# Kernel tuning notes

Hardware: AMD Instinct MI355X
Metric: run time of the kernel (lower is better)

## Reference

```python
import jax, jax.numpy as jnp
import numpy as np

B, S, V, H = 32, 512, 32, 128
EPS = 1e-5

def _ln(h, w, b):
    m = jnp.mean(h, axis=-1, keepdims=True)
    var = jnp.mean((h - m) ** 2, axis=-1, keepdims=True)
    return (h - m) * jax.lax.rsqrt(var + EPS) * w + b

def setup_inputs() -> dict:
    key = jax.random.key(0)
    ks = jax.random.split(key, 24)
    n = lambda k, shp: jax.random.normal(k, shp, dtype=jnp.float32) * 0.05
    return {
        "x": jax.random.normal(ks[0], (B, S, V), dtype=jnp.float32),
        # flattened GRN (input_dim=V -> H)
        "fw1": n(ks[1], (H, V)), "fb1": jnp.zeros((H,), jnp.float32),
        "fw2": n(ks[2], (H, H)), "fb2": jnp.zeros((H,), jnp.float32),
        "fgw": n(ks[3], (H, H)), "fgb": jnp.zeros((H,), jnp.float32),
        "fsw": n(ks[4], (H, V)), "fsb": jnp.zeros((H,), jnp.float32),
        "flnw": jnp.ones((H,), jnp.float32), "flnb": jnp.zeros((H,), jnp.float32),
        # V per-variable GRNs (input_dim=1 -> H), stacked on leading V axis
        "vw1": n(ks[5], (V, H)), "vb1": jnp.zeros((V, H), jnp.float32),
        "vw2": n(ks[6], (V, H, H)), "vb2": jnp.zeros((V, H), jnp.float32),
        "vgw": n(ks[7], (V, H, H)), "vgb": jnp.zeros((V, H), jnp.float32),
        "vsw": n(ks[8], (V, H)), "vsb": jnp.zeros((V, H), jnp.float32),
        "vlnw": jnp.ones((V, H), jnp.float32), "vlnb": jnp.zeros((V, H), jnp.float32),
    }

def reference(x, fw1, fb1, fw2, fb2, fgw, fgb, fsw, fsb, flnw, flnb,
              vw1, vb1, vw2, vb2, vgw, vgb, vsw, vsb, vlnw, vlnb):
    # ---- flattened GRN -> variable weights ----
    h = jax.nn.elu(jnp.einsum('bsv,hv->bsh', x, fw1) + fb1)
    h = jnp.einsum('bsh,kh->bsk', h, fw2) + fb2
    g = jax.nn.sigmoid(jnp.einsum('bsh,kh->bsk', h, fgw) + fgb)
    skip = jnp.einsum('bsv,hv->bsh', x, fsw) + fsb
    w_out = _ln(g * h + (1.0 - g) * skip, flnw, flnb)        # [B,S,H]
    weights = jax.nn.softmax(w_out[..., :V], axis=-1)        # [B,S,V]
    # ---- per-variable GRNs, batched over V ----
    xe = x[..., None]                                         # [B,S,V,1]
    hv = jax.nn.elu(xe * vw1 + vb1)                           # [B,S,V,H]
    hv = jnp.einsum('bsvh,vkh->bsvk', hv, vw2) + vb2
    gv = jax.nn.sigmoid(jnp.einsum('bsvh,vkh->bsvk', hv, vgw) + vgb)
    skipv = xe * vsw + vsb                                    # [B,S,V,H]
    vout = _ln(gv * hv + (1.0 - gv) * skipv, vlnw, vlnb)      # [B,S,V,H]
    # ---- softmax-weighted combination ----
    selected = jnp.einsum('bsvh,bsv->bsh', vout, weights)     # [B,S,H]
    return selected, weights
```

## Files before the change

### kernel.cpp

```cpp
#include <hip/hip_runtime.h>
#include <hip/hip_bf16.h>

typedef __bf16 bf16_t;
typedef __bf16 bf16x8 __attribute__((ext_vector_type(8)));
typedef float  f32x4  __attribute__((ext_vector_type(4)));

#define DEVFN static __device__ __forceinline__

constexpr int TOK   = 32 * 512;
constexpr int W_OFF = TOK * 128;

constexpr size_t WS_A_VW2 = 0;
constexpr size_t WS_A_WG2 = (size_t)1 << 20;
constexpr size_t WS_BG2   = (size_t)2 << 20;
constexpr size_t WS_A_FW2 = ((size_t)2 << 20) + (64u  << 10);
constexpr size_t WS_A_WG1 = ((size_t)2 << 20) + (128u << 10);
constexpr size_t WS_BG1   = ((size_t)2 << 20) + (192u << 10);
constexpr size_t WS_A_FW1 = ((size_t)2 << 20) + (224u << 10);
constexpr size_t WS_A_FSW = ((size_t)2 << 20) + (256u << 10);
constexpr size_t WS_PART  = (size_t)3 << 20;
constexpr size_t PART_SZ  = (size_t)TOK * 128 * 4;

DEVFN float eluf(float z)  { return z > 0.0f ? z : (__expf(z) - 1.0f); }
DEVFN float sigmf(float z) { return __builtin_amdgcn_rcpf(1.0f + __expf(-z)); }
DEVFN unsigned short f2bfu(float f){ bf16_t h = (bf16_t)f; return __builtin_bit_cast(unsigned short, h); }

DEVFN uint4 pack8(f32x4 a, f32x4 b){
  uint4 r;
  r.x = (unsigned)f2bfu(a[0]) | ((unsigned)f2bfu(a[1]) << 16);
  r.y = (unsigned)f2bfu(a[2]) | ((unsigned)f2bfu(a[3]) << 16);
  r.z = (unsigned)f2bfu(b[0]) | ((unsigned)f2bfu(b[1]) << 16);
  r.w = (unsigned)f2bfu(b[2]) | ((unsigned)f2bfu(b[3]) << 16);
  return r;
}
DEVFN f32x4 mfma16(bf16x8 a, bf16x8 b, f32x4 c){
  return __builtin_amdgcn_mfma_f32_16x16x32_bf16(a, b, c, 0, 0, 0);
}
DEVFN bf16x8 asbf(uint4 u){ return __builtin_bit_cast(bf16x8, u); }

__global__ void k0_prep(const float* __restrict__ fw1, const float* __restrict__ fw2,
                        const float* __restrict__ fgw, const float* __restrict__ fgb,
                        const float* __restrict__ fb2, const float* __restrict__ fsw,
                        const float* __restrict__ vw2, const float* __restrict__ vgw,
                        const float* __restrict__ vgb, const float* __restrict__ vb2,
                        unsigned char* __restrict__ ws)
{
  const int b = blockIdx.x, tid = threadIdx.x;
  if (b < 256){
    const int v  = b >> 3;
    const int k2 = (b & 7) * 16 + (tid >> 4);
    const int h0 = (tid & 15) * 8;
    const float* gw = vgw + ((size_t)v * 128 + k2) * 128;
    const float* w2 = vw2 + (size_t)v * 128 * 128;
    f32x4 a0 = {0,0,0,0}, a1 = {0,0,0,0};
    for (int k = 0; k < 128; ++k){
      float a = gw[k];
      f32x4 u = *(const f32x4*)(w2 + k*128 + h0);
      f32x4 w = *(const f32x4*)(w2 + k*128 + h0 + 4);
      #pragma unroll
      for (int e = 0; e < 4; ++e){ a0[e] = fmaf(a, u[e], a0[e]); a1[e] = fmaf(a, w[e], a1[e]); }
    }
    unsigned blk = (unsigned)(h0 >> 3) ^ (unsigned)(k2 & 7);
    *(uint4*)(ws + WS_A_WG2 + (size_t)v*32768 + (size_t)k2*256 + blk*16) = pack8(a0, a1);
    if ((b & 7) == 0 && tid < 128){
      const float* gr = vgw + ((size_t)v*128 + tid) * 128;
      const float* vb = vb2 + v*128;
      float s = vgb[v*128 + tid];
      for (int k = 0; k < 128; ++k) s = fmaf(gr[k], vb[k], s);
      ((float*)(ws + WS_BG2))[v*128 + tid] = s;
    }
  } else if (b < 288){
    const int v = b - 256;
    const int k = tid >> 1, hh = (tid & 1) * 64;
    const float* src = vw2 + ((size_t)v*128 + k) * 128;
    #pragma unroll
    for (int i = 0; i < 8; ++i){
      int h0 = hh + i*8;
      f32x4 a = *(const f32x4*)(src + h0);
      f32x4 c = *(const f32x4*)(src + h0 + 4);
      unsigned blk = (unsigned)(h0 >> 3) ^ (unsigned)(k & 7);
      *(uint4*)(ws + WS_A_VW2 + (size_t)v*32768 + (size_t)k*256 + blk*16) = pack8(a, c);
    }
  } else if (b < 296){
    const int k2 = (b - 288) * 16 + (tid >> 4);
    const int h0 = (tid & 15) * 8;
    const float* gw = fgw + (size_t)k2 * 128;
    f32x4 a0 = {0,0,0,0}, a1 = {0,0,0,0};
    for (int k = 0; k < 128; ++k){
      float a = gw[k];
      f32x4 u = *(const f32x4*)(fw2 + k*128 + h0);
      f32x4 w = *(const f32x4*)(fw2 + k*128 + h0 + 4);
      #pragma unroll
      for (int e = 0; e < 4; ++e){ a0[e] = fmaf(a, u[e], a0[e]); a1[e] = fmaf(a, w[e], a1[e]); }
    }
    unsigned blk = (unsigned)(h0 >> 3) ^ (unsigned)(k2 & 7);
    *(uint4*)(ws + WS_A_WG1 + (size_t)k2*256 + blk*16) = pack8(a0, a1);
    if (b == 288 && tid < 128){
      const float* gr = fgw + (size_t)tid * 128;
      float s = fgb[tid];
      for (int k = 0; k < 128; ++k) s = fmaf(gr[k], fb2[k], s);
      ((float*)(ws + WS_BG1))[tid] = s;
    }
  } else if (b == 296){
    const int k = tid >> 1, hh = (tid & 1) * 64;
    const float* src = fw2 + (size_t)k * 128;
    #pragma unroll
    for (int i = 0; i < 8; ++i){
      int h0 = hh + i*8;
      f32x4 a = *(const f32x4*)(src + h0);
      f32x4 c = *(const f32x4*)(src + h0 + 4);
      unsigned blk = (unsigned)(h0 >> 3) ^ (unsigned)(k & 7);
      *(uint4*)(ws + WS_A_FW2 + (size_t)k*256 + blk*16) = pack8(a, c);
    }
  } else if (b == 297){
    const int k = tid >> 1, v0 = (tid & 1) * 16;
    #pragma unroll
    for (int i = 0; i < 2; ++i){
      f32x4 a  = *(const f32x4*)(fw1 + k*32 + v0 + i*8);
      f32x4 c  = *(const f32x4*)(fw1 + k*32 + v0 + i*8 + 4);
      *(uint4*)(ws + WS_A_FW1 + (size_t)k*64 + (size_t)v0*2 + i*16) = pack8(a, c);
      f32x4 a2 = *(const f32x4*)(fsw + k*32 + v0 + i*8);
      f32x4 c2 = *(const f32x4*)(fsw + k*32 + v0 + i*8 + 4);
      *(uint4*)(ws + WS_A_FSW + (size_t)k*64 + (size_t)v0*2 + i*16) = pack8(a2, c2);
    }
  }
}

__global__ __launch_bounds__(256) void k1_flat(
  const float* __restrict__ x,   const float* __restrict__ fb1,
  const float* __restrict__ fb2, const float* __restrict__ fsb,
  const float* __restrict__ flnw,const float* __restrict__ flnb,
  const unsigned char* __restrict__ ws, float* __restrict__ out)
{
  __shared__ __align__(16) unsigned char ldsW[65536];
  __shared__ __align__(16) unsigned char ldsH[4][4096];
  const int tid = threadIdx.x;
  const int wid = tid >> 6, lane = tid & 63;
  const int tl = lane & 15, q = lane >> 4;
  const int t0 = blockIdx.x * 64;
  const int tw = t0 + wid * 16 + tl;

  {
    const uint4* s1 = (const uint4*)(ws + WS_A_FW2);
    const uint4* s2 = (const uint4*)(ws + WS_A_WG1);
    uint4* d1 = (uint4*)ldsW;
    uint4* d2 = (uint4*)(ldsW + 32768);
    #pragma unroll
    for (int i = 0; i < 8; ++i){ d1[tid + i*256] = s1[tid + i*256]; d2[tid + i*256] = s2[tid + i*256]; }
  }
  bf16x8 xf;
  {
    f32x4 a = *(const f32x4*)(x + (size_t)tw*32 + q*8);
    f32x4 c = *(const f32x4*)(x + (size_t)tw*32 + q*8 + 4);
    #pragma unroll
    for (int e = 0; e < 4; ++e){ xf[e] = (bf16_t)a[e]; xf[e+4] = (bf16_t)c[e]; }
  }
  __syncthreads();

  const unsigned swzt = (unsigned)(tl & 7) << 4;
  #pragma unroll
  for (int mt = 0; mt < 8; ++mt){
    const int row = mt*16 + tl;
    uint4 araw = *(const uint4*)(ws + WS_A_FW1 + (size_t)row*64 + q*16);
    f32x4 acc = *(const f32x4*)(fb1 + mt*16 + q*4);
    acc = mfma16(asbf(araw), xf, acc);
    ushort4 hb;
    hb.x = f2bfu(eluf(acc[0])); hb.y = f2bfu(eluf(acc[1]));
    hb.z = f2bfu(eluf(acc[2])); hb.w = f2bfu(eluf(acc[3]));
    *(ushort4*)(ldsH[wid] + (unsigned)tl*256 + (((unsigned)(mt*32 + q*8)) ^ swzt)) = hb;
  }
  bf16x8 h1f[4];
  #pragma unroll
  for (int kb = 0; kb < 4; ++kb)
    h1f[kb] = asbf(*(const uint4*)(ldsH[wid] + (unsigned)tl*256 + (((unsigned)(kb*64 + q*16)) ^ swzt)));

  f32x4 wo[8];
  const float* bg1p = (const float*)(ws + WS_BG1);
  #pragma unroll
  for (int mt = 0; mt < 8; ++mt){
    const int row = mt*16 + tl;
    const uint4* aw = (const uint4*)(ldsW + (size_t)row*256);
    const uint4* ag = (const uint4*)(ldsW + 32768 + (size_t)row*256);
    const unsigned rsw = (unsigned)(row & 7);
    f32x4 h2 = *(const f32x4*)(fb2 + mt*16 + q*4);
    f32x4 gp = *(const f32x4*)(bg1p + mt*16 + q*4);
    #pragma unroll
    for (int kb = 0; kb < 4; ++kb){
      unsigned blk = (unsigned)(kb*4 + q) ^ rsw;
      h2 = mfma16(asbf(aw[blk]), h1f[kb], h2);
      gp = mfma16(asbf(ag[blk]), h1f[kb], gp);
    }
    uint4 asr = *(const uint4*)(ws + WS_A_FSW + (size_t)row*64 + q*16);
    f32x4 sk = *(const f32x4*)(fsb + mt*16 + q*4);
    sk = mfma16(asbf(asr), xf, sk);
    #pragma unroll
    for (int r = 0; r < 4; ++r){
      float g = sigmf(gp[r]);
      wo[mt][r] = sk[r] + g * (h2[r] - sk[r]);
    }
  }
  float sm = 0.f, sq = 0.f;
  #pragma unroll
  for (int mt = 0; mt < 8; ++mt)
  #pragma unroll
  for (int r = 0; r < 4; ++r){ float p = wo[mt][r]; sm += p; sq = fmaf(p, p, sq); }
  sm += __shfl_xor(sm, 16); sm += __shfl_xor(sm, 32);
  sq += __shfl_xor(sq, 16); sq += __shfl_xor(sq, 32);
  const float mean = sm * (1.f/128.f);
  const float var  = sq * (1.f/128.f) - mean*mean;
  const float rs   = __builtin_amdgcn_rsqf(var + 1e-5f);
  float wv[8];
  #pragma unroll
  for (int mt = 0; mt < 2; ++mt){
    f32x4 lw = *(const f32x4*)(flnw + mt*16 + q*4);
    f32x4 lb = *(const f32x4*)(flnb + mt*16 + q*4);
    #pragma unroll
    for (int r = 0; r < 4; ++r) wv[mt*4+r] = (wo[mt][r] - mean) * rs * lw[r] + lb[r];
  }
  float mx = wv[0];
  #pragma unroll
  for (int j = 1; j < 8; ++j) mx = fmaxf(mx, wv[j]);
  mx = fmaxf(mx, __shfl_xor(mx, 16)); mx = fmaxf(mx, __shfl_xor(mx, 32));
  float se = 0.f;
  #pragma unroll
  for (int j = 0; j < 8; ++j){ wv[j] = __expf(wv[j] - mx); se += wv[j]; }
  se += __shfl_xor(se, 16); se += __shfl_xor(se, 32);
  const float inv = __builtin_amdgcn_rcpf(se);
  #pragma unroll
  for (int mt = 0; mt < 2; ++mt)
  #pragma unroll
  for (int r = 0; r < 4; ++r)
    out[(size_t)W_OFF + (size_t)tw*32 + mt*16 + q*4 + r] = wv[mt*4+r] * inv;
}

__global__ __launch_bounds__(512, 2) void k2_main(
  const float* __restrict__ x,   const float* __restrict__ vw1,
  const float* __restrict__ vb1, const float* __restrict__ vb2,
  const float* __restrict__ vsw, const float* __restrict__ vsb,
  const float* __restrict__ vlnw,const float* __restrict__ vlnb,
  const unsigned char* __restrict__ ws, float* __restrict__ out,
  float* __restrict__ part, int nvg)
{
  __shared__ __align__(16) uint4 slab[4096];
  const int tid = threadIdx.x;
  const int wid = tid >> 6, lane = tid & 63;
  const int tl = lane & 15, q = lane >> 4;
  const int bid = blockIdx.x;
  const int c   = bid & 127;
  const int g   = bid >> 7;
  const int VPG = 32 / nvg;
  const int vbase = g * VPG;
  const int t0 = ((c & 7) * 16 + (c >> 3)) * 128;
  const int ta = t0 + wid * 16 + tl;
  const float* bg2p = (const float*)(ws + WS_BG2);
  float* __restrict__ dst = (g == nvg - 1) ? out : (part + (size_t)g * TOK * 128);

  {
    const uint4* sa = (const uint4*)(ws + WS_A_VW2 + (size_t)vbase*32768);
    const uint4* sg = (const uint4*)(ws + WS_A_WG2 + (size_t)vbase*32768);
    #pragma unroll
    for (int i = 0; i < 4; ++i) slab[tid + i*512] = sa[tid + i*512];
    #pragma unroll
    for (int i = 0; i < 4; ++i) slab[2048 + tid + i*512] = sg[tid + i*512];
  }
  __syncthreads();

  f32x4 sel[8];
  #pragma unroll
  for (int mt = 0; mt < 8; ++mt) sel[mt] = (f32x4){0.f,0.f,0.f,0.f};

  for (int vi = 0; vi < VPG; ++vi){
    const int v = vbase + vi;
    const float xv0 = x[(size_t)ta*32 + v];
    const float wt0 = out[(size_t)W_OFF + (size_t)ta*32 + v];

    bf16x8 bf0[4];
    #pragma unroll
    for (int kb = 0; kb < 4; ++kb){
      const float* wp = vw1 + v*128 + kb*32 + q*8;
      const float* bp = vb1 + v*128 + kb*32 + q*8;
      f32x4 w0v = *(const f32x4*)wp, w1v = *(const f32x4*)(wp + 4);
      f32x4 b0v = *(const f32x4*)bp, b1v = *(const f32x4*)(bp + 4);
      bf16x8 f0;
      #pragma unroll
      for (int e = 0; e < 4; ++e){
        f0[e]   = (bf16_t)eluf(fmaf(xv0, w0v[e], b0v[e]));
        f0[e+4] = (bf16_t)eluf(fmaf(xv0, w1v[e], b1v[e]));
      }
      bf0[kb] = f0;
    }

    f32x4 pre[8];
    #pragma unroll
    for (int mt = 0; mt < 8; ++mt){
      const int row = mt*16 + tl;
      const uint4* arow = slab + row*16;
      const uint4* grow = slab + 2048 + row*16;
      const unsigned rsw = (unsigned)(row & 7);
      f32x4 h0 = *(const f32x4*)(vb2 + v*128 + mt*16 + q*4);
      f32x4 g0 = *(const f32x4*)(bg2p + v*128 + mt*16 + q*4);
      #pragma unroll
      for (int kb = 0; kb < 4; ++kb){
        const unsigned blk = (unsigned)(kb*4 + q) ^ rsw;
        h0 = mfma16(asbf(arow[blk]), bf0[kb], h0);
        g0 = mfma16(asbf(grow[blk]), bf0[kb], g0);
      }
      f32x4 sw_ = *(const f32x4*)(vsw + v*128 + mt*16 + q*4);
      f32x4 sb_ = *(const f32x4*)(vsb + v*128 + mt*16 + q*4);
      #pragma unroll
      for (int r = 0; r < 4; ++r){
        float sk0 = fmaf(xv0, sw_[r], sb_[r]);
        pre[mt][r] = sk0 + sigmf(g0[r]) * (h0[r] - sk0);
      }
    }

    {
      float sm = 0.f, sq = 0.f;
      #pragma unroll
      for (int mt = 0; mt < 8; ++mt)
      #pragma unroll
      for (int r = 0; r < 4; ++r){ float p = pre[mt][r]; sm += p; sq = fmaf(p, p, sq); }
      sm += __shfl_xor(sm, 16); sm += __shfl_xor(sm, 32);
      sq += __shfl_xor(sq, 16); sq += __shfl_xor(sq, 32);
      const float mean = sm * (1.f/128.f);
      const float var  = sq * (1.f/128.f) - mean*mean;
      const float rsq  = __builtin_amdgcn_rsqf(var + 1e-5f);
      const float c1   = wt0 * rsq;
      #pragma unroll
      for (int mt = 0; mt < 8; ++mt){
        f32x4 lw = *(const f32x4*)(vlnw + v*128 + mt*16 + q*4);
        f32x4 lb = *(const f32x4*)(vlnb + v*128 + mt*16 + q*4);
        #pragma unroll
        for (int r = 0; r < 4; ++r)
          sel[mt][r] = fmaf((pre[mt][r] - mean) * lw[r], c1,
                            fmaf(wt0, lb[r], sel[mt][r]));
      }
    }

    __syncthreads();
    if (vi + 1 < VPG){
      const uint4* sa = (const uint4*)(ws + WS_A_VW2 + (size_t)(v+1)*32768);
      const uint4* sg = (const uint4*)(ws + WS_A_WG2 + (size_t)(v+1)*32768);
      #pragma unroll
      for (int i = 0; i < 4; ++i) slab[tid + i*512] = sa[tid + i*512];
      #pragma unroll
      for (int i = 0; i < 4; ++i) slab[2048 + tid + i*512] = sg[tid + i*512];
      __syncthreads();
    }
  }

  #pragma unroll
  for (int mt = 0; mt < 8; ++mt)
    *(f32x4*)(dst + (size_t)ta*128 + mt*16 + q*4) = sel[mt];
}

__global__ __launch_bounds__(256) void k3_reduce(float* __restrict__ out,
                                                 const float* __restrict__ part,
                                                 int nparts)
{
  const size_t idx = (size_t)blockIdx.x * 256 + threadIdx.x;
  f32x4 s = ((const f32x4*)out)[idx];
  for (int g = 0; g < nparts; ++g){
    f32x4 p = ((const f32x4*)part)[(size_t)g * TOK * 32 + idx];
    #pragma unroll
    for (int r = 0; r < 4; ++r) s[r] += p[r];
  }
  ((f32x4*)out)[idx] = s;
}

extern "C" void kernel_launch(void* const* d_in, const int* in_sizes, int n_in,
                              void* d_out, int out_size, void* d_ws, size_t ws_size,
                              hipStream_t stream)
{
  (void)in_sizes; (void)n_in; (void)out_size;
  const float* x    = (const float*)d_in[0];
  const float* fw1  = (const float*)d_in[1];
  const float* fb1  = (const float*)d_in[2];
  const float* fw2  = (const float*)d_in[3];
  const float* fb2  = (const float*)d_in[4];
  const float* fgw  = (const float*)d_in[5];
  const float* fgb  = (const float*)d_in[6];
  const float* fsw  = (const float*)d_in[7];
  const float* fsb  = (const float*)d_in[8];
  const float* flnw = (const float*)d_in[9];
  const float* flnb = (const float*)d_in[10];
  const float* vw1  = (const float*)d_in[11];
  const float* vb1  = (const float*)d_in[12];
  const float* vw2  = (const float*)d_in[13];
  const float* vb2  = (const float*)d_in[14];
  const float* vgw  = (const float*)d_in[15];
  const float* vgb  = (const float*)d_in[16];
  const float* vsw  = (const float*)d_in[17];
  const float* vsb  = (const float*)d_in[18];
  const float* vlnw = (const float*)d_in[19];
  const float* vlnb = (const float*)d_in[20];
  float* out = (float*)d_out;
  unsigned char* ws = (unsigned char*)d_ws;
  float* part = (float*)(ws + WS_PART);

  k0_prep<<<298, 256, 0, stream>>>(fw1, fw2, fgw, fgb, fb2, fsw, vw2, vgw, vgb, vb2, ws);
  k1_flat<<<256, 256, 0, stream>>>(x, fb1, fb2, fsb, flnw, flnb, ws, out);

  if (ws_size >= WS_PART + 3 * PART_SZ){
    k2_main<<<512, 512, 0, stream>>>(x, vw1, vb1, vb2, vsw, vsb, vlnw, vlnb,
                                     ws, out, part, 4);
    k3_reduce<<<2048, 256, 0, stream>>>(out, part, 3);
  } else if (ws_size >= WS_PART + PART_SZ){
    k2_main<<<256, 512, 0, stream>>>(x, vw1, vb1, vb2, vsw, vsb, vlnw, vlnb,
                                     ws, out, part, 2);
    k3_reduce<<<2048, 256, 0, stream>>>(out, part, 1);
  } else {
    k2_main<<<128, 512, 0, stream>>>(x, vw1, vb1, vb2, vsw, vsb, vlnw, vlnb,
                                     ws, out, part, 1);
  }
}
```

Before: 141.3 us.

## Double-buffer weight slabs via async global-to-LDS loads, process two token tiles per wave

```diff
diff --git a/kernel.cpp b/kernel.cpp
--- a/kernel.cpp
+++ b/kernel.cpp
@@ -233,7 +233,7 @@
     out[(size_t)W_OFF + (size_t)tw*32 + mt*16 + q*4 + r] = wv[mt*4+r] * inv;
 }
 
-__global__ __launch_bounds__(512, 2) void k2_main(
+__global__ __launch_bounds__(512, 1) void k2_main(
   const float* __restrict__ x,   const float* __restrict__ vw1,
   const float* __restrict__ vb1, const float* __restrict__ vb2,
   const float* __restrict__ vsw, const float* __restrict__ vsb,
@@ -241,117 +241,138 @@
   const unsigned char* __restrict__ ws, float* __restrict__ out,
   float* __restrict__ part, int nvg)
 {
-  __shared__ __align__(16) uint4 slab[4096];
+  __shared__ __align__(16) uint4 slab[8192];
   const int tid = threadIdx.x;
   const int wid = tid >> 6, lane = tid & 63;
   const int tl = lane & 15, q = lane >> 4;
   const int bid = blockIdx.x;
-  const int c   = bid & 127;
-  const int g   = bid >> 7;
+  const int c   = bid & 63;
+  const int g   = bid >> 6;
   const int VPG = 32 / nvg;
   const int vbase = g * VPG;
-  const int t0 = ((c & 7) * 16 + (c >> 3)) * 128;
-  const int ta = t0 + wid * 16 + tl;
+  const int t0 = ((c & 7) * 8 + (c >> 3)) * 256;
+  const int ta = t0 + wid * 32 + tl, tb = ta + 16;
   const float* bg2p = (const float*)(ws + WS_BG2);
   float* __restrict__ dst = (g == nvg - 1) ? out : (part + (size_t)g * TOK * 128);
 
-  {
-    const uint4* sa = (const uint4*)(ws + WS_A_VW2 + (size_t)vbase*32768);
-    const uint4* sg = (const uint4*)(ws + WS_A_WG2 + (size_t)vbase*32768);
-    #pragma unroll
-    for (int i = 0; i < 4; ++i) slab[tid + i*512] = sa[tid + i*512];
-    #pragma unroll
-    for (int i = 0; i < 4; ++i) slab[2048 + tid + i*512] = sg[tid + i*512];
-  }
+  auto stage = [&](int buf, int v){
+    const uint4* sa = (const uint4*)(ws + WS_A_VW2 + (size_t)v*32768) + tid;
+    const uint4* sg = (const uint4*)(ws + WS_A_WG2 + (size_t)v*32768) + tid;
+    uint4* da = slab + buf*4096 + tid;
+    uint4* dg = slab + buf*4096 + 2048 + tid;
+    #pragma unroll
+    for (int i = 0; i < 4; ++i)
+      __builtin_amdgcn_global_load_lds(
+        (const __attribute__((address_space(1))) void*)(sa + i*512),
+        (__attribute__((address_space(3))) void*)(da + i*512), 16, 0, 0);
+    #pragma unroll
+    for (int i = 0; i < 4; ++i)
+      __builtin_amdgcn_global_load_lds(
+        (const __attribute__((address_space(1))) void*)(sg + i*512),
+        (__attribute__((address_space(3))) void*)(dg + i*512), 16, 0, 0);
+  };
+
+  stage(0, vbase);
   __syncthreads();
 
-  f32x4 sel[8];
-  #pragma unroll
-  for (int mt = 0; mt < 8; ++mt) sel[mt] = (f32x4){0.f,0.f,0.f,0.f};
-
+  f32x4 sel[2][8];
+  #pragma unroll
+  for (int mt = 0; mt < 8; ++mt){ sel[0][mt] = (f32x4){0,0,0,0}; sel[1][mt] = (f32x4){0,0,0,0}; }
+
+  int cur = 0;
   for (int vi = 0; vi < VPG; ++vi){
     const int v = vbase + vi;
+    if (vi + 1 < VPG) stage(cur ^ 1, v + 1);
+
     const float xv0 = x[(size_t)ta*32 + v];
+    const float xv1 = x[(size_t)tb*32 + v];
     const float wt0 = out[(size_t)W_OFF + (size_t)ta*32 + v];
-
-    bf16x8 bf0[4];
+    const float wt1 = out[(size_t)W_OFF + (size_t)tb*32 + v];
+
+    bf16x8 bf0[4], bf1[4];
     #pragma unroll
     for (int kb = 0; kb < 4; ++kb){
       const float* wp = vw1 + v*128 + kb*32 + q*8;
       const float* bp = vb1 + v*128 + kb*32 + q*8;
       f32x4 w0v = *(const f32x4*)wp, w1v = *(const f32x4*)(wp + 4);
       f32x4 b0v = *(const f32x4*)bp, b1v = *(const f32x4*)(bp + 4);
-      bf16x8 f0;
+      bf16x8 f0, f1;
       #pragma unroll
       for (int e = 0; e < 4; ++e){
         f0[e]   = (bf16_t)eluf(fmaf(xv0, w0v[e], b0v[e]));
         f0[e+4] = (bf16_t)eluf(fmaf(xv0, w1v[e], b1v[e]));
+        f1[e]   = (bf16_t)eluf(fmaf(xv1, w0v[e], b0v[e]));
+        f1[e+4] = (bf16_t)eluf(fmaf(xv1, w1v[e], b1v[e]));
       }
-      bf0[kb] = f0;
-    }
-
-    f32x4 pre[8];
+      bf0[kb] = f0; bf1[kb] = f1;
+    }
+
+    const uint4* sl = slab + cur*4096;
+    f32x4 pre[8][2];
     #pragma unroll
     for (int mt = 0; mt < 8; ++mt){
       const int row = mt*16 + tl;
-      const uint4* arow = slab + row*16;
-      const uint4* grow = slab + 2048 + row*16;
+      const uint4* arow = sl + row*16;
+      const uint4* grow = sl + 2048 + row*16;
       const unsigned rsw = (unsigned)(row & 7);
-      f32x4 h0 = *(const f32x4*)(vb2 + v*128 + mt*16 + q*4);
-      f32x4 g0 = *(const f32x4*)(bg2p + v*128 + mt*16 + q*4);
+      f32x4 bini = *(const f32x4*)(vb2 + v*128 + mt*16 + q*4);
+      f32x4 gini = *(const f32x4*)(bg2p + v*128 + mt*16 + q*4);
+      f32x4 h0 = bini, h1 = bini, g0 = gini, g1 = gini;
       #pragma unroll
       for (int kb = 0; kb < 4; ++kb){
         const unsigned blk = (unsigned)(kb*4 + q) ^ rsw;
-        h0 = mfma16(asbf(arow[blk]), bf0[kb], h0);
-        g0 = mfma16(asbf(grow[blk]), bf0[kb], g0);
+        bf16x8 a = asbf(arow[blk]);
+        bf16x8 gg = asbf(grow[blk]);
+        h0 = mfma16(a, bf0[kb], h0);
+        h1 = mfma16(a, bf1[kb], h1);
+        g0 = mfma16(gg, bf0[kb], g0);
+        g1 = mfma16(gg, bf1[kb], g1);
       }
       f32x4 sw_ = *(const f32x4*)(vsw + v*128 + mt*16 + q*4);
       f32x4 sb_ = *(const f32x4*)(vsb + v*128 + mt*16 + q*4);
       #pragma unroll
       for (int r = 0; r < 4; ++r){
         float sk0 = fmaf(xv0, sw_[r], sb_[r]);
-        pre[mt][r] = sk0 + sigmf(g0[r]) * (h0[r] - sk0);
+        float sk1 = fmaf(xv1, sw_[r], sb_[r]);
+        pre[mt][0][r] = sk0 + sigmf(g0[r]) * (h0[r] - sk0);
+        pre[mt][1][r] = sk1 + sigmf(g1[r]) * (h1[r] - sk1);
       }
     }
 
-    {
+    #pragma unroll
+    for (int nt = 0; nt < 2; ++nt){
+      const float wt = nt ? wt1 : wt0;
       float sm = 0.f, sq = 0.f;
       #pragma unroll
       for (int mt = 0; mt < 8; ++mt)
       #pragma unroll
-      for (int r = 0; r < 4; ++r){ float p = pre[mt][r]; sm += p; sq = fmaf(p, p, sq); }
+      for (int r = 0; r < 4; ++r){ float p = pre[mt][nt][r]; sm += p; sq = fmaf(p, p, sq); }
       sm += __shfl_xor(sm, 16); sm += __shfl_xor(sm, 32);
       sq += __shfl_xor(sq, 16); sq += __shfl_xor(sq, 32);
       const float mean = sm * (1.f/128.f);
       const float var  = sq * (1.f/128.f) - mean*mean;
       const float rsq  = __builtin_amdgcn_rsqf(var + 1e-5f);
-      const float c1   = wt0 * rsq;
+      const float c1   = wt * rsq;
       #pragma unroll
       for (int mt = 0; mt < 8; ++mt){
         f32x4 lw = *(const f32x4*)(vlnw + v*128 + mt*16 + q*4);
         f32x4 lb = *(const f32x4*)(vlnb + v*128 + mt*16 + q*4);
         #pragma unroll
         for (int r = 0; r < 4; ++r)
-          sel[mt][r] = fmaf((pre[mt][r] - mean) * lw[r], c1,
-                            fmaf(wt0, lb[r], sel[mt][r]));
+          sel[nt][mt][r] = fmaf((pre[mt][nt][r] - mean) * lw[r], c1,
+                                fmaf(wt, lb[r], sel[nt][mt][r]));
       }
     }
 
     __syncthreads();
-    if (vi + 1 < VPG){
-      const uint4* sa = (const uint4*)(ws + WS_A_VW2 + (size_t)(v+1)*32768);
-      const uint4* sg = (const uint4*)(ws + WS_A_WG2 + (size_t)(v+1)*32768);
-      #pragma unroll
-      for (int i = 0; i < 4; ++i) slab[tid + i*512] = sa[tid + i*512];
-      #pragma unroll
-      for (int i = 0; i < 4; ++i) slab[2048 + tid + i*512] = sg[tid + i*512];
-      __syncthreads();
-    }
-  }
-
-  #pragma unroll
-  for (int mt = 0; mt < 8; ++mt)
-    *(f32x4*)(dst + (size_t)ta*128 + mt*16 + q*4) = sel[mt];
+    cur ^= 1;
+  }
+
+  #pragma unroll
+  for (int mt = 0; mt < 8; ++mt){
+    *(f32x4*)(dst + (size_t)ta*128 + mt*16 + q*4) = sel[0][mt];
+    *(f32x4*)(dst + (size_t)tb*128 + mt*16 + q*4) = sel[1][mt];
+  }
 }
 
 __global__ __launch_bounds__(256) void k3_reduce(float* __restrict__ out,
@@ -402,15 +423,15 @@
   k1_flat<<<256, 256, 0, stream>>>(x, fb1, fb2, fsb, flnw, flnb, ws, out);
 
   if (ws_size >= WS_PART + 3 * PART_SZ){
-    k2_main<<<512, 512, 0, stream>>>(x, vw1, vb1, vb2, vsw, vsb, vlnw, vlnb,
+    k2_main<<<256, 512, 0, stream>>>(x, vw1, vb1, vb2, vsw, vsb, vlnw, vlnb,
                                      ws, out, part, 4);
     k3_reduce<<<2048, 256, 0, stream>>>(out, part, 3);
   } else if (ws_size >= WS_PART + PART_SZ){
-    k2_main<<<256, 512, 0, stream>>>(x, vw1, vb1, vb2, vsw, vsb, vlnw, vlnb,
+    k2_main<<<128, 512, 0, stream>>>(x, vw1, vb1, vb2, vsw, vsb, vlnw, vlnb,
                                      ws, out, part, 2);
     k3_reduce<<<2048, 256, 0, stream>>>(out, part, 1);
   } else {
-    k2_main<<<128, 512, 0, stream>>>(x, vw1, vb1, vb2, vsw, vsb, vlnw, vlnb,
-                                     ws, out, part, 1);
-  }
-}
+    k2_main<<<64, 512, 0, stream>>>(x, vw1, vb1, vb2, vsw, vsb, vlnw, vlnb,
+                                    ws, out, part, 1);
+  }
+}
```

Measured after the change: 148.1 us. 4.8% more time.

## Double-buffer vw2 slab via async global-to-LDS loads; read gate weights from global

Applied to the files above, without the earlier changes.

```diff
diff --git a/kernel.cpp b/kernel.cpp
--- a/kernel.cpp
+++ b/kernel.cpp
@@ -60,8 +60,10 @@
       #pragma unroll
       for (int e = 0; e < 4; ++e){ a0[e] = fmaf(a, u[e], a0[e]); a1[e] = fmaf(a, w[e], a1[e]); }
     }
-    unsigned blk = (unsigned)(h0 >> 3) ^ (unsigned)(k2 & 7);
-    *(uint4*)(ws + WS_A_WG2 + (size_t)v*32768 + (size_t)k2*256 + blk*16) = pack8(a0, a1);
+    const int mt = k2 >> 4, tl = k2 & 15;
+    const int kb = h0 >> 5, qq = (h0 >> 3) & 3;
+    *(uint4*)(ws + WS_A_WG2 + (size_t)v*32768 +
+              (size_t)(((mt*4 + kb)*64) + qq*16 + tl)*16) = pack8(a0, a1);
     if ((b & 7) == 0 && tid < 128){
       const float* gr = vgw + ((size_t)v*128 + tid) * 128;
       const float* vb = vb2 + v*128;
@@ -241,7 +243,7 @@
   const unsigned char* __restrict__ ws, float* __restrict__ out,
   float* __restrict__ part, int nvg)
 {
-  __shared__ __align__(16) uint4 slab[4096];
+  __shared__ __align__(16) uint4 slabA[4096];
   const int tid = threadIdx.x;
   const int wid = tid >> 6, lane = tid & 63;
   const int tl = lane & 15, q = lane >> 4;
@@ -255,22 +257,28 @@
   const float* bg2p = (const float*)(ws + WS_BG2);
   float* __restrict__ dst = (g == nvg - 1) ? out : (part + (size_t)g * TOK * 128);
 
-  {
-    const uint4* sa = (const uint4*)(ws + WS_A_VW2 + (size_t)vbase*32768);
-    const uint4* sg = (const uint4*)(ws + WS_A_WG2 + (size_t)vbase*32768);
-    #pragma unroll
-    for (int i = 0; i < 4; ++i) slab[tid + i*512] = sa[tid + i*512];
-    #pragma unroll
-    for (int i = 0; i < 4; ++i) slab[2048 + tid + i*512] = sg[tid + i*512];
-  }
+  auto stageA = [&](int buf, int v){
+    const uint4* sa = (const uint4*)(ws + WS_A_VW2 + (size_t)v*32768) + tid;
+    uint4* da = slabA + buf*2048 + tid;
+    #pragma unroll
+    for (int i = 0; i < 4; ++i)
+      __builtin_amdgcn_global_load_lds(
+        (const __attribute__((address_space(1))) void*)(sa + i*512),
+        (__attribute__((address_space(3))) void*)(da + i*512), 16, 0, 0);
+  };
+
+  stageA(0, vbase);
   __syncthreads();
 
   f32x4 sel[8];
   #pragma unroll
   for (int mt = 0; mt < 8; ++mt) sel[mt] = (f32x4){0.f,0.f,0.f,0.f};
 
+  int cur = 0;
   for (int vi = 0; vi < VPG; ++vi){
     const int v = vbase + vi;
+    if (vi + 1 < VPG) stageA(cur ^ 1, v + 1);
+
     const float xv0 = x[(size_t)ta*32 + v];
     const float wt0 = out[(size_t)W_OFF + (size_t)ta*32 + v];
 
@@ -290,20 +298,25 @@
       bf0[kb] = f0;
     }
 
+    const uint4* sl = slabA + cur*2048;
+    const uint4* gv = (const uint4*)(ws + WS_A_WG2 + (size_t)v*32768);
     f32x4 pre[8];
     #pragma unroll
     for (int mt = 0; mt < 8; ++mt){
       const int row = mt*16 + tl;
-      const uint4* arow = slab + row*16;
-      const uint4* grow = slab + 2048 + row*16;
+      const uint4* arow = sl + row*16;
       const unsigned rsw = (unsigned)(row & 7);
       f32x4 h0 = *(const f32x4*)(vb2 + v*128 + mt*16 + q*4);
       f32x4 g0 = *(const f32x4*)(bg2p + v*128 + mt*16 + q*4);
+      bf16x8 gg[4];
+      #pragma unroll
+      for (int kb = 0; kb < 4; ++kb)
+        gg[kb] = asbf(gv[(mt*4 + kb)*64 + q*16 + tl]);
       #pragma unroll
       for (int kb = 0; kb < 4; ++kb){
         const unsigned blk = (unsigned)(kb*4 + q) ^ rsw;
         h0 = mfma16(asbf(arow[blk]), bf0[kb], h0);
-        g0 = mfma16(asbf(grow[blk]), bf0[kb], g0);
+        g0 = mfma16(gg[kb], bf0[kb], g0);
       }
       f32x4 sw_ = *(const f32x4*)(vsw + v*128 + mt*16 + q*4);
       f32x4 sb_ = *(const f32x4*)(vsb + v*128 + mt*16 + q*4);
@@ -338,15 +351,7 @@
     }
 
     __syncthreads();
-    if (vi + 1 < VPG){
-      const uint4* sa = (const uint4*)(ws + WS_A_VW2 + (size_t)(v+1)*32768);
-      const uint4* sg = (const uint4*)(ws + WS_A_WG2 + (size_t)(v+1)*32768);
-      #pragma unroll
-      for (int i = 0; i < 4; ++i) slab[tid + i*512] = sa[tid + i*512];
-      #pragma unroll
-      for (int i = 0; i < 4; ++i) slab[2048 + tid + i*512] = sg[tid + i*512];
-      __syncthreads();
-    }
+    cur ^= 1;
   }
 
   #pragma unroll
```

Measured after the change: 171.2 us. 21.2% more time.
